# Optimization experiments

Hardware: AMD Instinct MI355X
Metric: run time of the kernel (lower is better)

The kernel has to match this reference:

```python
import jax, jax.numpy as jnp
import numpy as np

NUM_DIRECTIONS = 64
NUM_STEPS = 64
D = 64
NEG_INF = -1e9  # matches the original's -inf sentinel of 1e9


def _sample_directions(n):
    # Mirrors WeightedEulerCurve._obtainDirection with np.random.seed(4)
    np.random.seed(4)
    out = []
    for _ in range(n):
        phi = np.random.uniform(0, np.pi * 2)
        costheta = np.random.uniform(-1, 1)
        theta = np.arccos(costheta)
        out.append([np.sin(theta) * np.cos(phi), np.sin(theta) * np.sin(phi), np.cos(theta)])
    return np.asarray(out, dtype=np.float32)


def setup_inputs() -> dict:
    key = jax.random.key(0)
    # strictly positive -> dense cubical complex (every voxel is a vertex,
    # every adjacent pair an edge, etc.), matching torch.nonzero on x>0
    x = jax.random.uniform(key, (D, D, D), dtype=jnp.float32) + 1e-3
    dirs = jnp.asarray(_sample_directions(NUM_DIRECTIONS))  # (K, 3)
    return {"x": x, "dirs": dirs}


def _pairmax(a, axis):
    n = a.shape[axis]
    return jnp.maximum(jax.lax.slice_in_dim(a, 0, n - 1, axis=axis),
                       jax.lax.slice_in_dim(a, 1, n, axis=axis))


def _curve_contrib(heights, vals, intervals):
    # heights: (K, N) per-direction simplex heights; vals: (N,) shared weights
    K = heights.shape[0]
    idx = jnp.argsort(heights, axis=-1)
    sorted_h = jnp.take_along_axis(heights, idx, axis=-1)
    sorted_v = jnp.take(vals, idx)                                    # (K, N)
    csum = jnp.concatenate([jnp.zeros((K, 1), heights.dtype),
                            jnp.cumsum(sorted_v, axis=-1)], axis=-1)  # (K, N+1)
    padded_h = jnp.concatenate([jnp.full((K, 1), NEG_INF, heights.dtype),
                                sorted_h], axis=-1)                   # (K, N+1)
    ptr = jax.vmap(lambda h: jnp.searchsorted(h, intervals, side='right'))(padded_h) - 1
    return jnp.take_along_axis(csum, ptr, axis=-1)                    # (K, num_intervals)


def _wect(x, dirs, num_steps):
    d = x.shape[0]
    K = dirs.shape[0]
    r = jnp.arange(d, dtype=x.dtype)
    d0, d1, d2 = dirs[:, 0], dirs[:, 1], dirs[:, 2]
    # vertex heights per direction: H[k,i,j,l] = d0*i + d1*j + d2*l
    H = (d0[:, None, None, None] * r[:, None, None]
         + d1[:, None, None, None] * r[None, :, None]
         + d2[:, None, None, None] * r[None, None, :])
    p0, p1, p2 = (jax.nn.relu(d0)[:, None], jax.nn.relu(d1)[:, None], jax.nn.relu(d2)[:, None])

    min_h = -(3.0 ** 0.5) * d
    dh = (-2.0 * min_h) / num_steps
    intervals = jnp.asarray(min_h + dh * np.arange(num_steps + 1), dtype=x.dtype)

    # vertices
    vh = H.reshape(K, -1)
    vv = x.reshape(-1)

    # edges along each axis: max over the 2 endpoints -> base height + relu(d_axis)
    eh = jnp.concatenate([
        H[:, :-1].reshape(K, -1) + p0,
        H[:, :, :-1].reshape(K, -1) + p1,
        H[:, :, :, :-1].reshape(K, -1) + p2], axis=1)
    ev = jnp.concatenate([
        _pairmax(x, 0).reshape(-1),
        _pairmax(x, 1).reshape(-1),
        _pairmax(x, 2).reshape(-1)])

    # squares spanning axis pairs (1,2), (0,2), (0,1): max over 4 corners
    sh = jnp.concatenate([
        H[:, :, :-1, :-1].reshape(K, -1) + p1 + p2,
        H[:, :-1, :, :-1].reshape(K, -1) + p0 + p2,
        H[:, :-1, :-1, :].reshape(K, -1) + p0 + p1], axis=1)
    sv = jnp.concatenate([
        _pairmax(_pairmax(x, 1), 2).reshape(-1),
        _pairmax(_pairmax(x, 0), 2).reshape(-1),
        _pairmax(_pairmax(x, 0), 1).reshape(-1)])

    # cubes: max over 8 corners
    ch = H[:, :-1, :-1, :-1].reshape(K, -1) + p0 + p1 + p2
    cv = _pairmax(_pairmax(_pairmax(x, 0), 1), 2).reshape(-1)

    v = _curve_contrib(vh, vv, intervals)
    e = _curve_contrib(eh, ev, intervals)
    s = _curve_contrib(sh, sv, intervals)
    c = _curve_contrib(ch, cv, intervals)
    return v - e + s - c  # (K, num_steps + 1)


def reference(x, dirs):
    return _wect(x, dirs, NUM_STEPS)
```

## Files before the change

kernel.cpp:

```cpp
#include <hip/hip_runtime.h>
#include <math.h>

#define NDIRS 64
#define NBIN 65
#define WIN 21
#define WROW (WIN*64)
#define STAGEF 512
#define THREADS 512
#define WPB 8
#define NBLK 512
#define ROWF (NDIRS*NBIN)
#define MROWS 64

static constexpr float INV = 0.28867513459481287f;

__global__ __launch_bounds__(THREADS) void wect_hist(
    const float* __restrict__ x, const float* __restrict__ dirs,
    float* __restrict__ accum) {
  __shared__ float histw[WPB * WROW];
  __shared__ float stage[WPB * STAGEF];
  __shared__ int   b0s[WPB * 64];
  const int tid = threadIdx.x;
  const int lane = tid & 63;
  const int wid  = tid >> 6;

  float4* h4 = (float4*)histw;
  for (int idx = tid; idx < WPB * WROW / 4; idx += THREADS)
    h4[idx] = make_float4(0.f, 0.f, 0.f, 0.f);
  __syncthreads();

  const float D0 = dirs[3*lane+0] * INV;
  const float D1 = dirs[3*lane+1] * INV;
  const float D2 = dirs[3*lane+2] * INV;
  const float Q1 = fmaxf(D0, 0.f);
  const float Q2 = fmaxf(D1, 0.f);
  const float Q3 = fmaxf(D2, 0.f);
  const float Q4 = Q2 + Q3;
  const float Q5 = Q1 + Q3;
  const float Q6 = Q1 + Q2;
  const float Q7 = Q1 + Q2 + Q3;

  float* __restrict__ myhw = histw + wid * WROW + lane;
  float4* __restrict__ mystage = (float4*)(stage + wid * STAGEF);

  {
    const int strip = blockIdx.x * WPB + wid;
    const int i = strip >> 6, j = strip & 63;
    const int l = lane;
    const float* p = x + (strip << 6) + l;
    const int dL = (l < 63) ? 1 : 0;
    const int dJ = (j < 63) ? 64 : 0;
    const int dI = (i < 63) ? 4096 : 0;
    const bool iv = dI != 0, jv = dJ != 0, lv = dL != 0;

    const float x000 = p[0],       x001 = p[dL];
    const float x010 = p[dJ],      x011 = p[dJ+dL];
    const float x100 = p[dI],      x101 = p[dI+dL];
    const float x110 = p[dI+dJ],   x111 = p[dI+dJ+dL];

    const float e0m = fmaxf(x000, x100);
    const float e1m = fmaxf(x000, x010);
    const float e2m = fmaxf(x000, x001);
    const float s12 = fmaxf(fmaxf(e1m, x001), x011);
    const float s02 = fmaxf(fmaxf(e0m, x001), x101);
    const float s01 = fmaxf(fmaxf(e0m, x010), x110);
    const float cc  = fmaxf(fmaxf(s01, fmaxf(x001, x101)), fmaxf(x011, x111));

    const float v1 = iv ? -e0m : 0.f;
    const float v2 = jv ? -e1m : 0.f;
    const float v3 = lv ? -e2m : 0.f;
    const float v4 = (jv && lv) ? s12 : 0.f;
    const float v5 = (iv && lv) ? s02 : 0.f;
    const float v6 = (iv && jv) ? s01 : 0.f;
    const float v7 = (iv && jv && lv) ? -cc : 0.f;
    const float T  = x000 + v1+v2+v3+v4+v5+v6+v7;

    mystage[2*lane]     = make_float4(T,  v1, v2, v3);
    mystage[2*lane + 1] = make_float4(v4, v5, v6, v7);

    const float u0 = (float)i * D0 + (float)j * D1;

    const float u63 = fmaf(63.f, D2, u0);
    const int ib0  = (int)ceilf(u0);
    const int ib63 = (int)ceilf(u63);
    const int wbase = min(ib0, ib63);
    b0s[wid*64 + lane] = wbase + 32;

    #pragma unroll 8
    for (int t = 0; t < 64; ++t) {
      const float4 A = mystage[2*t];
      const float4 B = mystage[2*t + 1];
      const float u  = fmaf((float)t, D2, u0);
      const float bf = ceilf(u);
      const float fr = bf - u;
      const int   w  = (int)bf - wbase;
      float S = 0.f;
      S += (Q1 > fr) ? A.y : 0.f;
      S += (Q2 > fr) ? A.z : 0.f;
      S += (Q3 > fr) ? A.w : 0.f;
      S += (Q4 > fr) ? B.x : 0.f;
      S += (Q5 > fr) ? B.y : 0.f;
      S += (Q6 > fr) ? B.z : 0.f;
      S += (Q7 > fr) ? B.w : 0.f;
      float* a = myhw + (w << 6);
      const float r0 = a[0], r1 = a[64];
      a[0]  = r0 + (A.x - S);
      a[64] = r1 + S;
    }
  }

  __syncthreads();
  float* __restrict__ obase = accum + blockIdx.x * ROWF;
  const int k = tid & 63;
  const int b0 = b0s[0*64 + k], b1 = b0s[1*64 + k],
            b2 = b0s[2*64 + k], b3 = b0s[3*64 + k],
            b4 = b0s[4*64 + k], b5 = b0s[5*64 + k],
            b6 = b0s[6*64 + k], b7 = b0s[7*64 + k];
  for (int z = tid; z < ROWF; z += THREADS) {
    const int c = z >> 6;
    float v = 0.f;
    int w;
    w = c - b0; if ((unsigned)w < WIN) v += histw[0*WROW + (w << 6) + k];
    w = c - b1; if ((unsigned)w < WIN) v += histw[1*WROW + (w << 6) + k];
    w = c - b2; if ((unsigned)w < WIN) v += histw[2*WROW + (w << 6) + k];
    w = c - b3; if ((unsigned)w < WIN) v += histw[3*WROW + (w << 6) + k];
    w = c - b4; if ((unsigned)w < WIN) v += histw[4*WROW + (w << 6) + k];
    w = c - b5; if ((unsigned)w < WIN) v += histw[5*WROW + (w << 6) + k];
    w = c - b6; if ((unsigned)w < WIN) v += histw[6*WROW + (w << 6) + k];
    w = c - b7; if ((unsigned)w < WIN) v += histw[7*WROW + (w << 6) + k];
    obase[z] = v;
  }
}

__global__ __launch_bounds__(256) void wect_reduceA(
    const float* __restrict__ accum, float* __restrict__ mid) {
  const int q = blockIdx.x * 256 + threadIdx.x;
  if (q >= MROWS * ROWF) return;
  const int g = q / ROWF, z = q - g * ROWF;
  float v = 0.f;
  #pragma unroll
  for (int m = 0; m < NBLK / MROWS; ++m)
    v += accum[(g * (NBLK / MROWS) + m) * ROWF + z];
  mid[g * ROWF + z] = v;
}

__global__ __launch_bounds__(512) void wect_scan(
    const float* __restrict__ mid, float* __restrict__ out) {
  __shared__ float red[8 * NBIN];
  __shared__ float s[NBIN];
  const int k = blockIdx.x, tid = threadIdx.x;
  for (int z = tid; z < 8 * NBIN; z += 512) {
    const int g = z / NBIN, c = z - g * NBIN;
    float v = 0.f;
    #pragma unroll
    for (int r = g; r < MROWS; r += 8) v += mid[r * ROWF + (c << 6) + k];
    red[z] = v;
  }
  __syncthreads();
  if (tid < NBIN) {
    float v = 0.f;
    #pragma unroll
    for (int gg = 0; gg < 8; ++gg) v += red[gg * NBIN + tid];
    s[tid] = v;
  }
  __syncthreads();
  for (int off = 1; off < NBIN; off <<= 1) {
    float a = 0.f;
    if (tid < NBIN && tid >= off) a = s[tid - off];
    __syncthreads();
    if (tid < NBIN && tid >= off) s[tid] += a;
    __syncthreads();
  }
  if (tid < NBIN) out[k * NBIN + tid] = s[tid];
}

extern "C" void kernel_launch(void* const* d_in, const int* in_sizes, int n_in,
                              void* d_out, int out_size, void* d_ws, size_t ws_size,
                              hipStream_t stream) {
  const float* x = (const float*)d_in[0];
  const float* dirs = (const float*)d_in[1];
  float* out = (float*)d_out;
  float* accum = (float*)d_ws;
  float* mid = accum + NBLK * ROWF;

  wect_hist<<<NBLK, THREADS, 0, stream>>>(x, dirs, accum);
  wect_reduceA<<<(MROWS * ROWF + 255) / 256, 256, 0, stream>>>(accum, mid);
  wect_scan<<<NDIRS, 512, 0, stream>>>(mid, out);
}
```

Baseline: 85.06 us.

## Process two strips per wave and drop intermediate reduction kernel

Each wave now handles two adjacent j-strips that share one histogram window, which halves the block count and the number of per-block partial histograms written to global memory. The separate reduceA pass is removed, and the scan kernel sums all 256 partial rows directly. The cost is less parallelism in the histogram kernel and a longer serial reduction loop per thread in the scan kernel. The shared window must also cover both strips' height ranges within WIN bins.

```diff
diff --git a/kernel.cpp b/kernel.cpp
--- a/kernel.cpp
+++ b/kernel.cpp
@@ -8,9 +8,10 @@
 #define STAGEF 512
 #define THREADS 512
 #define WPB 8
-#define NBLK 512
+#define SPW 2
+#define NBLK 256
 #define ROWF (NDIRS*NBIN)
-#define MROWS 64
+#define NROWS 256
 
 static constexpr float INV = 0.28867513459481287f;
 
@@ -43,9 +44,18 @@
   float* __restrict__ myhw = histw + wid * WROW + lane;
   float4* __restrict__ mystage = (float4*)(stage + wid * STAGEF);
 
-  {
-    const int strip = blockIdx.x * WPB + wid;
-    const int i = strip >> 6, j = strip & 63;
+  const int strip0 = (blockIdx.x * WPB + wid) * SPW;
+  const int i = strip0 >> 6, j0 = strip0 & 63;
+  const float u00 = (float)i * D0 + (float)j0 * D1;
+  const float u01 = u00 + D1;
+  const float e00 = fmaf(63.f, D2, u00);
+  const float e01 = fmaf(63.f, D2, u01);
+  const int wbase = (int)ceilf(fminf(fminf(u00, e00), fminf(u01, e01)));
+  b0s[wid*64 + lane] = wbase + 32;
+
+  for (int s = 0; s < SPW; ++s) {
+    const int strip = strip0 + s;
+    const int j = j0 + s;
     const int l = lane;
     const float* p = x + (strip << 6) + l;
     const int dL = (l < 63) ? 1 : 0;
@@ -78,13 +88,7 @@
     mystage[2*lane]     = make_float4(T,  v1, v2, v3);
     mystage[2*lane + 1] = make_float4(v4, v5, v6, v7);
 
-    const float u0 = (float)i * D0 + (float)j * D1;
-
-    const float u63 = fmaf(63.f, D2, u0);
-    const int ib0  = (int)ceilf(u0);
-    const int ib63 = (int)ceilf(u63);
-    const int wbase = min(ib0, ib63);
-    b0s[wid*64 + lane] = wbase + 32;
+    const float u0 = (s == 0) ? u00 : u01;
 
     #pragma unroll 8
     for (int t = 0; t < 64; ++t) {
@@ -132,28 +136,16 @@
   }
 }
 
-__global__ __launch_bounds__(256) void wect_reduceA(
-    const float* __restrict__ accum, float* __restrict__ mid) {
-  const int q = blockIdx.x * 256 + threadIdx.x;
-  if (q >= MROWS * ROWF) return;
-  const int g = q / ROWF, z = q - g * ROWF;
-  float v = 0.f;
-  #pragma unroll
-  for (int m = 0; m < NBLK / MROWS; ++m)
-    v += accum[(g * (NBLK / MROWS) + m) * ROWF + z];
-  mid[g * ROWF + z] = v;
-}
-
 __global__ __launch_bounds__(512) void wect_scan(
-    const float* __restrict__ mid, float* __restrict__ out) {
+    const float* __restrict__ accum, float* __restrict__ out) {
   __shared__ float red[8 * NBIN];
   __shared__ float s[NBIN];
   const int k = blockIdx.x, tid = threadIdx.x;
   for (int z = tid; z < 8 * NBIN; z += 512) {
     const int g = z / NBIN, c = z - g * NBIN;
     float v = 0.f;
-    #pragma unroll
-    for (int r = g; r < MROWS; r += 8) v += mid[r * ROWF + (c << 6) + k];
+    #pragma unroll 4
+    for (int r = g; r < NROWS; r += 8) v += accum[r * ROWF + (c << 6) + k];
     red[z] = v;
   }
   __syncthreads();
@@ -181,9 +173,7 @@
   const float* dirs = (const float*)d_in[1];
   float* out = (float*)d_out;
   float* accum = (float*)d_ws;
-  float* mid = accum + NBLK * ROWF;
 
   wect_hist<<<NBLK, THREADS, 0, stream>>>(x, dirs, accum);
-  wect_reduceA<<<(MROWS * ROWF + 255) / 256, 256, 0, stream>>>(accum, mid);
-  wect_scan<<<NDIRS, 512, 0, stream>>>(mid, out);
+  wect_scan<<<NDIRS, 512, 0, stream>>>(accum, out);
 }
```

Measured after the change: 99.10 us. 16.5% more time.

## Restructure cross-block reduction into per-bin column sum and serial scan

Applied to the files above, without the earlier changes.

Replaces the two-stage reduction (64 intermediate rows, then a per-direction reduce and shared-memory scan) with a single column-sum kernel that has one block per bin, each summing all 512 partial histograms, followed by a tiny 64-thread serial prefix scan. This removes the intermediate buffer write and read and the barrier-heavy log-step scan. In exchange the column sum runs on only 65 blocks, so the 8.5 MB partial buffer is read with less parallelism, and the scan runs as a single small wave.

```diff
diff --git a/kernel.cpp b/kernel.cpp
--- a/kernel.cpp
+++ b/kernel.cpp
@@ -10,7 +10,6 @@
 #define WPB 8
 #define NBLK 512
 #define ROWF (NDIRS*NBIN)
-#define MROWS 64
 
 static constexpr float INV = 0.28867513459481287f;
 
@@ -132,46 +131,36 @@
   }
 }
 
-__global__ __launch_bounds__(256) void wect_reduceA(
-    const float* __restrict__ accum, float* __restrict__ mid) {
-  const int q = blockIdx.x * 256 + threadIdx.x;
-  if (q >= MROWS * ROWF) return;
-  const int g = q / ROWF, z = q - g * ROWF;
-  float v = 0.f;
-  #pragma unroll
-  for (int m = 0; m < NBLK / MROWS; ++m)
-    v += accum[(g * (NBLK / MROWS) + m) * ROWF + z];
-  mid[g * ROWF + z] = v;
+__global__ __launch_bounds__(512) void wect_colsum(
+    const float* __restrict__ accum, float* __restrict__ cs) {
+  __shared__ float part[8 * 64];
+  const int c = blockIdx.x;
+  const int k = threadIdx.x & 63;
+  const int w = threadIdx.x >> 6;
+  const float* __restrict__ base = accum + (c << 6) + k;
+  float acc = 0.f;
+  #pragma unroll 8
+  for (int m = 0; m < NBLK / 8; ++m)
+    acc += base[(w + (m << 3)) * ROWF];
+  part[(w << 6) + k] = acc;
+  __syncthreads();
+  if (w == 0) {
+    float t = 0.f;
+    #pragma unroll
+    for (int g = 0; g < 8; ++g) t += part[(g << 6) + k];
+    cs[(c << 6) + k] = t;
+  }
 }
 
-__global__ __launch_bounds__(512) void wect_scan(
-    const float* __restrict__ mid, float* __restrict__ out) {
-  __shared__ float red[8 * NBIN];
-  __shared__ float s[NBIN];
-  const int k = blockIdx.x, tid = threadIdx.x;
-  for (int z = tid; z < 8 * NBIN; z += 512) {
-    const int g = z / NBIN, c = z - g * NBIN;
-    float v = 0.f;
-    #pragma unroll
-    for (int r = g; r < MROWS; r += 8) v += mid[r * ROWF + (c << 6) + k];
-    red[z] = v;
+__global__ __launch_bounds__(64) void wect_scan(
+    const float* __restrict__ cs, float* __restrict__ out) {
+  const int k = threadIdx.x;
+  float s = 0.f;
+  #pragma unroll 5
+  for (int c = 0; c < NBIN; ++c) {
+    s += cs[(c << 6) + k];
+    out[k * NBIN + c] = s;
   }
-  __syncthreads();
-  if (tid < NBIN) {
-    float v = 0.f;
-    #pragma unroll
-    for (int gg = 0; gg < 8; ++gg) v += red[gg * NBIN + tid];
-    s[tid] = v;
-  }
-  __syncthreads();
-  for (int off = 1; off < NBIN; off <<= 1) {
-    float a = 0.f;
-    if (tid < NBIN && tid >= off) a = s[tid - off];
-    __syncthreads();
-    if (tid < NBIN && tid >= off) s[tid] += a;
-    __syncthreads();
-  }
-  if (tid < NBIN) out[k * NBIN + tid] = s[tid];
 }
 
 extern "C" void kernel_launch(void* const* d_in, const int* in_sizes, int n_in,
@@ -181,9 +170,9 @@
   const float* dirs = (const float*)d_in[1];
   float* out = (float*)d_out;
   float* accum = (float*)d_ws;
-  float* mid = accum + NBLK * ROWF;
+  float* cs = accum + NBLK * ROWF;
 
   wect_hist<<<NBLK, THREADS, 0, stream>>>(x, dirs, accum);
-  wect_reduceA<<<(MROWS * ROWF + 255) / 256, 256, 0, stream>>>(accum, mid);
-  wect_scan<<<NDIRS, 512, 0, stream>>>(mid, out);
+  wect_colsum<<<NBIN, 512, 0, stream>>>(accum, cs);
+  wect_scan<<<1, 64, 0, stream>>>(cs, out);
 }
```

Measured after the change: 84.83 us. Within noise of the previous version (-0.3%).
